# Kernel tuning notes

Measured on AMD Instinct MI355X. Metric: run time of the kernel, lower is better.

The kernel has to match this reference:

```python
import jax, jax.numpy as jnp
import numpy as np

# Static config mirroring init_kwargs
N, C, H, W = 2, 10, 30, 30
PAD = 4                    # pad_size
HL = WL = 1 + 2 * PAD      # 9x9 local window
MAXH = MAXW = 10           # max_height / max_width
L = MAXH * MAXW            # tokens per pixel sequence = 100
D = C + 1                  # d_model = 11 (color channels + pad indicator)
EPS = 1e-5


def setup_inputs() -> dict:
    key = jax.random.key(0)
    ks = jax.random.split(key, 7)
    # one-hot ARC-style grid: each pixel is one of C colors
    classes = jax.random.randint(ks[0], (N, H, W), 0, C)
    x = jax.nn.one_hot(classes, C, dtype=jnp.float32).transpose(0, 3, 1, 2)  # [N,C,H,W]
    s = 0.1
    w_in = jax.random.normal(ks[1], (3 * D, D), dtype=jnp.float32) * s   # in_proj_weight
    w_out = jax.random.normal(ks[2], (D, D), dtype=jnp.float32) * s     # out_proj
    w_ff1 = jax.random.normal(ks[3], (1, D), dtype=jnp.float32) * s     # linear1 (D->1)
    w_ff2 = jax.random.normal(ks[4], (D, 1), dtype=jnp.float32) * s     # linear2 (1->D)
    ln1_g = jnp.ones((D,), dtype=jnp.float32)
    ln2_g = jnp.ones((D,), dtype=jnp.float32)
    return {"x": x, "w_in": w_in, "w_out": w_out, "w_ff1": w_ff1,
            "w_ff2": w_ff2, "ln1_g": ln1_g, "ln2_g": ln2_g}


def _layernorm(x, g):
    m = jnp.mean(x, axis=-1, keepdims=True)
    v = jnp.var(x, axis=-1, keepdims=True)
    return (x - m) / jnp.sqrt(v + EPS) * g


def reference(x, w_in, w_out, w_ff1, w_ff2, ln1_g, ln2_g):
    # pad colors with pad_value=0, pad-indicator channel with 1 in the border
    xp = jnp.pad(x, ((0, 0), (0, 0), (PAD, PAD), (PAD, PAD)))
    ind = jnp.pad(jnp.zeros((N, 1, H, W), x.dtype),
                  ((0, 0), (0, 0), (PAD, PAD), (PAD, PAD)), constant_values=1.0)
    xa = jnp.concatenate([xp, ind], axis=1).transpose(0, 2, 3, 1)  # [N,Hp,Wp,D]

    # im2col: 9x9 window around every pixel
    ii = jnp.arange(H)[:, None] + jnp.arange(HL)[None, :]  # [H,HL]
    jj = jnp.arange(W)[:, None] + jnp.arange(WL)[None, :]  # [W,WL]
    patches = xa[:, ii[:, None, :, None], jj[None, :, None, :], :]   # [N,H,W,HL,WL,D]
    patches = patches.transpose(0, 1, 2, 5, 3, 4)                    # [N,H,W,D,HL,WL]
    # embed window into max_height x max_width canvas (fill = pad_value = 0)
    patches = jnp.pad(patches, ((0, 0),) * 4 + ((0, MAXH - HL), (0, MAXW - WL)))
    seq = patches.reshape(N * H * W, D, L).transpose(0, 2, 1)        # [B,L,D]

    mask_inf = jnp.all(seq == 0, axis=2)               # [B,L] key padding mask
    mask0 = (seq[:, :, -1:] == 1).astype(seq.dtype)    # [B,L,1] border-padding gate

    # --- TransformerEncoderLayer (post-norm, bias=False, eval/no-dropout) ---
    qkv = seq @ w_in.T                                 # [B,L,3D]
    q, k, v = jnp.split(qkv, 3, axis=-1)
    # nhead = D, head_dim = 1, scale = 1/sqrt(1) = 1 -> per-channel outer products
    scores = jnp.einsum('bqd,bkd->bdqk', q, k)         # [B,D,L,L]
    scores = jnp.where(mask_inf[:, None, None, :], -1e9, scores)
    attn = jax.nn.softmax(scores, axis=-1)
    ao = jnp.einsum('bdqk,bkd->bqd', attn, v) @ w_out.T
    h = _layernorm(seq + ao, ln1_g)
    ff = jax.nn.relu(h @ w_ff1.T) @ w_ff2.T            # D -> 1 -> D
    h = _layernorm(h + ff, ln2_g)

    # softmax over color channels, zero out everywhere except padded border tokens
    colored = jax.nn.softmax(h[:, :, :-1], axis=2) * mask0
    out = (seq[:, :, :-1] + colored).transpose(0, 2, 1)  # [B,C,L]
    return out
```

## Files before the change

### kernel.cpp

```cpp
#include <hip/hip_runtime.h>

#define NB   2
#define CC   10
#define HH   30
#define WW   30
#define PADR 4
#define DD   11
#define NPIX (NB*HH*WW)

__global__ __launch_bounds__(256) void pve_fused(
    const float* __restrict__ x,
    const float* __restrict__ w_in,
    const float* __restrict__ w_out,
    const float* __restrict__ w_ff1,
    const float* __restrict__ w_ff2,
    const float* __restrict__ ln1g,
    const float* __restrict__ ln2g,
    float* __restrict__ out)
{
    __shared__ float E[121];
    __shared__ float EV[121];
    __shared__ float WO[121];
    __shared__ float G1[11], G2[11], F1[11], F2[11];
    __shared__ float cntf[11];
    __shared__ float smvS[10];
    volatile __shared__ float aoS[16];
    __shared__ unsigned char chs[100];

    const int t = threadIdx.x;
    const int pix = blockIdx.x;
    const int n  = pix / (HH * WW);
    const int rm = pix % (HH * WW);
    const int i0 = rm / WW, j0 = rm % WW;

    if (t < 121) {
        const int d = t / 11, c = t % 11;
        const float Q = w_in[d * DD + 10];
        const float K = w_in[(DD + d) * DD + c];
        const float V = w_in[(2 * DD + d) * DD + c];
        const float e = __expf(Q * K);
        E[t] = e; EV[t] = e * V; WO[t] = w_out[t];
    }
    if (t < 11) {
        G1[t] = ln1g[t]; G2[t] = ln2g[t];
        F1[t] = w_ff1[t]; F2[t] = w_ff2[t];
    }

    if (t >= 128 && t < 192) {
        const int lane = t - 128;
        unsigned int pk0 = 0, pk1 = 0, pk2 = 0;
        for (int l = lane; l < 100; l += 64) {
            const int ph = l / 10, pw = l % 10;
            unsigned int c = 255;
            if (ph < 9 && pw < 9) {
                const int r  = i0 + ph - PADR;
                const int cc = j0 + pw - PADR;
                c = 10;
                if (r >= 0 && r < HH && cc >= 0 && cc < WW) {
                    const float* xp = x + n * CC * HH * WW + r * WW + cc;
                    int cls = 10;
                    #pragma unroll
                    for (int k = CC - 1; k >= 0; k--) {
                        if (xp[k * HH * WW] > 0.5f) cls = k;
                    }
                    c = (unsigned int)cls;
                }
                const unsigned int inc = 1u << ((c & 3) * 8);
                if (c < 4) pk0 += inc; else if (c < 8) pk1 += inc; else pk2 += inc;
            }
            chs[l] = (unsigned char)c;
        }
        #pragma unroll
        for (int m = 1; m < 64; m <<= 1) {
            pk0 += __shfl_xor(pk0, m, 64);
            pk1 += __shfl_xor(pk1, m, 64);
            pk2 += __shfl_xor(pk2, m, 64);
        }
        if (lane < 11) {
            const unsigned int pk = (lane < 4) ? pk0 : ((lane < 8) ? pk1 : pk2);
            cntf[lane] = (float)((pk >> ((lane & 3) * 8)) & 0xFFu);
        }
    }
    __syncthreads();

    if (t < 16) {
        const int g = t;
        const int d = (g < 11) ? g : 0;

        float s1 = 0.f, s2 = 0.f;
        #pragma unroll
        for (int c = 0; c < 11; c++) {
            const float cn = cntf[c];
            s1 += cn * E[d * 11 + c];
            s2 += cn * EV[d * 11 + c];
        }
        const float ao = s2 / s1;

        aoS[g] = ao;
        float h = 0.f;
        #pragma unroll
        for (int j = 0; j < 11; j++)
            h += WO[d * 11 + j] * aoS[j];
        if (g == 10) h += 1.0f;
        if (g >= 11) h = 0.f;

        float s = h;
        #pragma unroll
        for (int m = 1; m < 16; m <<= 1) s += __shfl_xor(s, m, 16);
        float mean = s * (1.f / 11.f);
        float dv = (g < 11) ? (h - mean) : 0.f;
        float sq = dv * dv;
        #pragma unroll
        for (int m = 1; m < 16; m <<= 1) sq += __shfl_xor(sq, m, 16);
        const float hb = dv * rsqrtf(sq * (1.f / 11.f) + 1e-5f) * G1[d];

        float f = hb * F1[d];
        #pragma unroll
        for (int m = 1; m < 16; m <<= 1) f += __shfl_xor(f, m, 16);
        f = fmaxf(f, 0.f);
        float h2 = hb + f * F2[d];
        if (g >= 11) h2 = 0.f;

        s = h2;
        #pragma unroll
        for (int m = 1; m < 16; m <<= 1) s += __shfl_xor(s, m, 16);
        mean = s * (1.f / 11.f);
        dv = (g < 11) ? (h2 - mean) : 0.f;
        sq = dv * dv;
        #pragma unroll
        for (int m = 1; m < 16; m <<= 1) sq += __shfl_xor(sq, m, 16);
        const float hc = dv * rsqrtf(sq * (1.f / 11.f) + 1e-5f) * G2[d];

        float mv = (g < 10) ? hc : -1e30f;
        #pragma unroll
        for (int m = 1; m < 16; m <<= 1) mv = fmaxf(mv, __shfl_xor(mv, m, 16));
        const float ex = (g < 10) ? __expf(hc - mv) : 0.f;
        float den = ex;
        #pragma unroll
        for (int m = 1; m < 16; m <<= 1) den += __shfl_xor(den, m, 16);
        if (g < 10) smvS[g] = ex / den;
    }
    __syncthreads();

    if (t < 250) {
        const int idx = t * 4;
        const int c   = idx / 100;
        const int l0  = idx - c * 100;
        const uchar4 c4 = *reinterpret_cast<const uchar4*>(chs + l0);
        const float sv = smvS[c];
        float4 v4;
        v4.x = (c4.x == 255) ? 0.f : ((c4.x < 10) ? ((c == c4.x) ? 1.f : 0.f) : sv);
        v4.y = (c4.y == 255) ? 0.f : ((c4.y < 10) ? ((c == c4.y) ? 1.f : 0.f) : sv);
        v4.z = (c4.z == 255) ? 0.f : ((c4.z < 10) ? ((c == c4.z) ? 1.f : 0.f) : sv);
        v4.w = (c4.w == 255) ? 0.f : ((c4.w < 10) ? ((c == c4.w) ? 1.f : 0.f) : sv);
        reinterpret_cast<float4*>(out + (size_t)pix * 1000)[t] = v4;
    }
}

extern "C" void kernel_launch(void* const* d_in, const int* in_sizes, int n_in,
                              void* d_out, int out_size, void* d_ws, size_t ws_size,
                              hipStream_t stream) {
    const float* x     = (const float*)d_in[0];
    const float* w_in  = (const float*)d_in[1];
    const float* w_out = (const float*)d_in[2];
    const float* w_ff1 = (const float*)d_in[3];
    const float* w_ff2 = (const float*)d_in[4];
    const float* ln1g  = (const float*)d_in[5];
    const float* ln2g  = (const float*)d_in[6];
    float* out = (float*)d_out;

    pve_fused<<<NPIX, 256, 0, stream>>>(x, w_in, w_out, w_ff1, w_ff2,
                                        ln1g, ln2g, out);
}
```

Baseline: 72.93 us.

## Shrink block to one wavefront and keep weight tables in registers

Launches 64 threads per pixel instead of 256, so one wavefront does the window classification, the attention/LN math and the output writes in loops. Each lane now loads its weight row into registers and computes the exp tables itself, replacing the shared-memory staging. The two layernorm reductions are merged into one pass using the sum/sum-of-squares variance, and the softmax max-subtraction is removed. This cuts block overhead and shared traffic, at the cost of redundant weight loads per lane and less stable variance and exp arithmetic.

After: 73.54 us. Within noise of the previous version (+0.8%).

```diff
diff --git a/kernel.cpp b/kernel.cpp
--- a/kernel.cpp
+++ b/kernel.cpp
@@ -8,7 +8,7 @@
 #define DD   11
 #define NPIX (NB*HH*WW)
 
-__global__ __launch_bounds__(256) void pve_fused(
+__global__ __launch_bounds__(64) void pve_fused(
     const float* __restrict__ x,
     const float* __restrict__ w_in,
     const float* __restrict__ w_out,
@@ -18,38 +18,36 @@
     const float* __restrict__ ln2g,
     float* __restrict__ out)
 {
-    __shared__ float E[121];
-    __shared__ float EV[121];
-    __shared__ float WO[121];
-    __shared__ float G1[11], G2[11], F1[11], F2[11];
     __shared__ float cntf[11];
+    volatile __shared__ float aoS[16];
     __shared__ float smvS[10];
-    volatile __shared__ float aoS[16];
     __shared__ unsigned char chs[100];
 
-    const int t = threadIdx.x;
+    const int t   = threadIdx.x;
     const int pix = blockIdx.x;
-    const int n  = pix / (HH * WW);
-    const int rm = pix % (HH * WW);
-    const int i0 = rm / WW, j0 = rm % WW;
+    const int n   = pix / (HH * WW);
+    const int rm  = pix % (HH * WW);
+    const int i0  = rm / WW, j0 = rm % WW;
 
-    if (t < 121) {
-        const int d = t / 11, c = t % 11;
-        const float Q = w_in[d * DD + 10];
-        const float K = w_in[(DD + d) * DD + c];
-        const float V = w_in[(2 * DD + d) * DD + c];
-        const float e = __expf(Q * K);
-        E[t] = e; EV[t] = e * V; WO[t] = w_out[t];
+    const int g = t & 15;
+    const int d = (g < 11) ? g : 0;
+
+    const float Q  = w_in[d * DD + 10];
+    float Krow[11], Vrow[11], Wrow[11];
+    #pragma unroll
+    for (int c = 0; c < 11; c++) {
+        Krow[c] = w_in[(DD + d) * DD + c];
+        Vrow[c] = w_in[(2 * DD + d) * DD + c];
+        Wrow[c] = w_out[d * DD + c];
     }
-    if (t < 11) {
-        G1[t] = ln1g[t]; G2[t] = ln2g[t];
-        F1[t] = w_ff1[t]; F2[t] = w_ff2[t];
-    }
+    const float g1 = ln1g[d], g2 = ln2g[d];
+    const float f1 = w_ff1[d], f2 = w_ff2[d];
 
-    if (t >= 128 && t < 192) {
-        const int lane = t - 128;
-        unsigned int pk0 = 0, pk1 = 0, pk2 = 0;
-        for (int l = lane; l < 100; l += 64) {
+    unsigned int pk0 = 0, pk1 = 0, pk2 = 0;
+    #pragma unroll
+    for (int it = 0; it < 2; ++it) {
+        const int l = t + it * 64;
+        if (l < 100) {
             const int ph = l / 10, pw = l % 10;
             unsigned int c = 255;
             if (ph < 9 && pw < 9) {
@@ -70,29 +68,35 @@
             }
             chs[l] = (unsigned char)c;
         }
-        #pragma unroll
-        for (int m = 1; m < 64; m <<= 1) {
-            pk0 += __shfl_xor(pk0, m, 64);
-            pk1 += __shfl_xor(pk1, m, 64);
-            pk2 += __shfl_xor(pk2, m, 64);
-        }
-        if (lane < 11) {
-            const unsigned int pk = (lane < 4) ? pk0 : ((lane < 8) ? pk1 : pk2);
-            cntf[lane] = (float)((pk >> ((lane & 3) * 8)) & 0xFFu);
-        }
+    }
+
+    float ec[11], ev[11];
+    #pragma unroll
+    for (int c = 0; c < 11; c++) {
+        const float e = __expf(Q * Krow[c]);
+        ec[c] = e;
+        ev[c] = e * Vrow[c];
+    }
+
+    #pragma unroll
+    for (int m = 1; m < 64; m <<= 1) {
+        pk0 += __shfl_xor(pk0, m, 64);
+        pk1 += __shfl_xor(pk1, m, 64);
+        pk2 += __shfl_xor(pk2, m, 64);
+    }
+    if (t < 11) {
+        const unsigned int pk = (t < 4) ? pk0 : ((t < 8) ? pk1 : pk2);
+        cntf[t] = (float)((pk >> ((t & 3) * 8)) & 0xFFu);
     }
     __syncthreads();
 
-    if (t < 16) {
-        const int g = t;
-        const int d = (g < 11) ? g : 0;
-
+    {
         float s1 = 0.f, s2 = 0.f;
         #pragma unroll
         for (int c = 0; c < 11; c++) {
             const float cn = cntf[c];
-            s1 += cn * E[d * 11 + c];
-            s2 += cn * EV[d * 11 + c];
+            s1 += cn * ec[c];
+            s2 += cn * ev[c];
         }
         const float ao = s2 / s1;
 
@@ -100,60 +104,62 @@
         float h = 0.f;
         #pragma unroll
         for (int j = 0; j < 11; j++)
-            h += WO[d * 11 + j] * aoS[j];
+            h += Wrow[j] * aoS[j];
         if (g == 10) h += 1.0f;
         if (g >= 11) h = 0.f;
 
-        float s = h;
+        float s = h, sq = h * h;
         #pragma unroll
-        for (int m = 1; m < 16; m <<= 1) s += __shfl_xor(s, m, 16);
-        float mean = s * (1.f / 11.f);
-        float dv = (g < 11) ? (h - mean) : 0.f;
-        float sq = dv * dv;
-        #pragma unroll
-        for (int m = 1; m < 16; m <<= 1) sq += __shfl_xor(sq, m, 16);
-        const float hb = dv * rsqrtf(sq * (1.f / 11.f) + 1e-5f) * G1[d];
+        for (int m = 1; m < 16; m <<= 1) {
+            s  += __shfl_xor(s,  m, 16);
+            sq += __shfl_xor(sq, m, 16);
+        }
+        const float mean1 = s * (1.f / 11.f);
+        const float var1  = sq * (1.f / 11.f) - mean1 * mean1;
+        float dv = (g < 11) ? (h - mean1) : 0.f;
+        const float hb = dv * rsqrtf(var1 + 1e-5f) * g1;
 
-        float f = hb * F1[d];
+        float f = hb * f1;
         #pragma unroll
         for (int m = 1; m < 16; m <<= 1) f += __shfl_xor(f, m, 16);
         f = fmaxf(f, 0.f);
-        float h2 = hb + f * F2[d];
+        float h2 = hb + f * f2;
         if (g >= 11) h2 = 0.f;
 
-        s = h2;
+        s = h2; sq = h2 * h2;
         #pragma unroll
-        for (int m = 1; m < 16; m <<= 1) s += __shfl_xor(s, m, 16);
-        mean = s * (1.f / 11.f);
-        dv = (g < 11) ? (h2 - mean) : 0.f;
-        sq = dv * dv;
-        #pragma unroll
-        for (int m = 1; m < 16; m <<= 1) sq += __shfl_xor(sq, m, 16);
-        const float hc = dv * rsqrtf(sq * (1.f / 11.f) + 1e-5f) * G2[d];
+        for (int m = 1; m < 16; m <<= 1) {
+            s  += __shfl_xor(s,  m, 16);
+            sq += __shfl_xor(sq, m, 16);
+        }
+        const float mean2 = s * (1.f / 11.f);
+        const float var2  = sq * (1.f / 11.f) - mean2 * mean2;
+        dv = (g < 11) ? (h2 - mean2) : 0.f;
+        const float hc = dv * rsqrtf(var2 + 1e-5f) * g2;
 
-        float mv = (g < 10) ? hc : -1e30f;
-        #pragma unroll
-        for (int m = 1; m < 16; m <<= 1) mv = fmaxf(mv, __shfl_xor(mv, m, 16));
-        const float ex = (g < 10) ? __expf(hc - mv) : 0.f;
+        const float ex = (g < 10) ? __expf(hc) : 0.f;
         float den = ex;
         #pragma unroll
         for (int m = 1; m < 16; m <<= 1) den += __shfl_xor(den, m, 16);
-        if (g < 10) smvS[g] = ex / den;
+        if (t < 10) smvS[t] = ex / den;
     }
     __syncthreads();
 
-    if (t < 250) {
-        const int idx = t * 4;
-        const int c   = idx / 100;
-        const int l0  = idx - c * 100;
-        const uchar4 c4 = *reinterpret_cast<const uchar4*>(chs + l0);
-        const float sv = smvS[c];
-        float4 v4;
-        v4.x = (c4.x == 255) ? 0.f : ((c4.x < 10) ? ((c == c4.x) ? 1.f : 0.f) : sv);
-        v4.y = (c4.y == 255) ? 0.f : ((c4.y < 10) ? ((c == c4.y) ? 1.f : 0.f) : sv);
-        v4.z = (c4.z == 255) ? 0.f : ((c4.z < 10) ? ((c == c4.z) ? 1.f : 0.f) : sv);
-        v4.w = (c4.w == 255) ? 0.f : ((c4.w < 10) ? ((c == c4.w) ? 1.f : 0.f) : sv);
-        reinterpret_cast<float4*>(out + (size_t)pix * 1000)[t] = v4;
+    #pragma unroll
+    for (int it = 0; it < 4; ++it) {
+        const int q = t + it * 64;
+        if (q < 250) {
+            const int c  = q / 25;
+            const int l0 = (q - c * 25) * 4;
+            const uchar4 c4 = *reinterpret_cast<const uchar4*>(chs + l0);
+            const float sv = smvS[c];
+            float4 v4;
+            v4.x = (c4.x == 255) ? 0.f : ((c4.x < 10) ? ((c == c4.x) ? 1.f : 0.f) : sv);
+            v4.y = (c4.y == 255) ? 0.f : ((c4.y < 10) ? ((c == c4.y) ? 1.f : 0.f) : sv);
+            v4.z = (c4.z == 255) ? 0.f : ((c4.z < 10) ? ((c == c4.z) ? 1.f : 0.f) : sv);
+            v4.w = (c4.w == 255) ? 0.f : ((c4.w < 10) ? ((c == c4.w) ? 1.f : 0.f) : sv);
+            reinterpret_cast<float4*>(out + (size_t)pix * 1000)[q] = v4;
+        }
     }
 }
 
@@ -169,6 +175,6 @@
     const float* ln2g  = (const float*)d_in[6];
     float* out = (float*)d_out;
 
-    pve_fused<<<NPIX, 256, 0, stream>>>(x, w_in, w_out, w_ff1, w_ff2,
-                                        ln1g, ln2g, out);
+    pve_fused<<<NPIX, 64, 0, stream>>>(x, w_in, w_out, w_ff1, w_ff2,
+                                       ln1g, ln2g, out);
 }
```
